# Optimization experiments

Measured on AMD Instinct MI355X. Metric: run time of the kernel, lower is better.

The kernel has to match this reference:

```python
import jax, jax.numpy as jnp
import numpy as np

HIDDEN = 2048
NUM_HEADS = 16
HEAD_DIM = HIDDEN // NUM_HEADS
WORLD_SIZE = 4
BATCH = 1
SEQ_SHARD = 2048


def setup_inputs() -> dict:
    key = jax.random.key(0)
    ks = jax.random.split(key, 9)
    s = 1.0 / np.sqrt(HIDDEN)
    return {
        'hidden_states': jax.random.normal(ks[0], (BATCH, SEQ_SHARD, HIDDEN), jnp.float32),
        'wq': jax.random.normal(ks[1], (HIDDEN, HIDDEN), jnp.float32) * s,
        'bq': jax.random.normal(ks[2], (HIDDEN,), jnp.float32) * s,
        'wk': jax.random.normal(ks[3], (HIDDEN, HIDDEN), jnp.float32) * s,
        'bk': jax.random.normal(ks[4], (HIDDEN,), jnp.float32) * s,
        'wv': jax.random.normal(ks[5], (HIDDEN, HIDDEN), jnp.float32) * s,
        'bv': jax.random.normal(ks[6], (HIDDEN,), jnp.float32) * s,
        'wo': jax.random.normal(ks[7], (HIDDEN, HIDDEN), jnp.float32) * s,
        'bo': jax.random.normal(ks[8], (HIDDEN,), jnp.float32) * s,
    }


def _ring_attention(q, k, v):
    # q, k, v: [B, H, S, D]. Simulation: every ring step receives the SAME
    # local KV shard (all_k_shards are clones of k), accumulated with
    # flash-style online softmax across WORLD_SIZE steps.
    B, H, S, D = q.shape
    scale = 1.0 / np.sqrt(D)
    output_acc = jnp.zeros_like(q)
    max_score = jnp.full((B, H, S, 1), -jnp.inf, dtype=q.dtype)
    sum_exp = jnp.zeros((B, H, S, 1), dtype=q.dtype)
    for _ in range(WORLD_SIZE):  # fixed small loop over ring steps
        scores = jnp.einsum('bhsd,bhtd->bhst', q, k) * scale  # [B,H,S,S]
        new_max = jnp.max(scores, axis=-1, keepdims=True)
        combined_max = jnp.maximum(max_score, new_max)
        old_scale = jnp.exp(max_score - combined_max)
        new_scale = jnp.exp(new_max - combined_max)
        new_exp = jnp.exp(scores - new_max)
        sum_exp = sum_exp * old_scale + jnp.sum(new_exp, axis=-1, keepdims=True) * new_scale
        output_acc = output_acc * old_scale + jnp.einsum('bhst,bhtd->bhsd', new_exp, v) * new_scale
        max_score = combined_max
    return output_acc / sum_exp


def reference(hidden_states, wq, bq, wk, bk, wv, bv, wo, bo):
    B, S, _ = hidden_states.shape
    # nn.Linear: y = x @ W^T + b
    q = hidden_states @ wq.T + bq
    k = hidden_states @ wk.T + bk
    v = hidden_states @ wv.T + bv
    split = lambda t: t.reshape(B, S, NUM_HEADS, HEAD_DIM).transpose(0, 2, 1, 3)
    attn = _ring_attention(split(q), split(k), split(v))  # [B,H,S,D]
    attn = attn.transpose(0, 2, 1, 3).reshape(B, S, HIDDEN)
    return attn @ wo.T + bo
```

## Files before the change

kernel.cpp:

```cpp
#include <hip/hip_runtime.h>
#include <hip/hip_bf16.h>
#include <stdint.h>

#define SEQ 2048
#define HID 2048
#define NH 16
#define HD 128
#define QSCALE_L2E 0.1275304429019769f

typedef __attribute__((ext_vector_type(4))) float f32x4;
typedef __attribute__((ext_vector_type(8))) short short8;
typedef __attribute__((ext_vector_type(4))) float f4;
typedef __attribute__((ext_vector_type(4))) unsigned short us4;

__device__ __forceinline__ unsigned short f2bu(float f) {
  union { float f; unsigned int u; } c; c.f = f;
  unsigned int u = c.u + 0x7fffu + ((c.u >> 16) & 1u);
  return (unsigned short)(u >> 16);
}

__device__ __forceinline__ unsigned short f2bu_fast(float f) {
  union { float f; unsigned int u; } c; c.f = f;
  return (unsigned short)((c.u + 0x8000u) >> 16);
}

__device__ __forceinline__ float b2f(unsigned short u) {
  union { unsigned int u; float f; } c; c.u = ((unsigned int)u) << 16; return c.f;
}

__device__ __forceinline__ float exp2fast(float x) {
  float r; asm("v_exp_f32 %0, %1" : "=v"(r) : "v"(x)); return r;
}

__device__ __forceinline__ void gload_lds16(const void* g, void* l) {
  __builtin_amdgcn_global_load_lds((const __attribute__((address_space(1))) void*)g,
                                   (__attribute__((address_space(3))) void*)l, 16, 0, 0);
}

#define BAR() __builtin_amdgcn_s_barrier()
#define LGKM0() do { asm volatile("s_waitcnt lgkmcnt(0)" ::: "memory"); __builtin_amdgcn_sched_barrier(0); } while (0)
#define VM6()   do { asm volatile("s_waitcnt vmcnt(6)"   ::: "memory"); __builtin_amdgcn_sched_barrier(0); } while (0)
#define VM8()   do { asm volatile("s_waitcnt vmcnt(8)"   ::: "memory"); __builtin_amdgcn_sched_barrier(0); } while (0)
#define VM0()   do { asm volatile("s_waitcnt vmcnt(0)"   ::: "memory"); __builtin_amdgcn_sched_barrier(0); } while (0)

__global__ __launch_bounds__(256) void cvt_kernel(
    const float* __restrict__ s0, const float* __restrict__ s1,
    const float* __restrict__ s2, const float* __restrict__ s3,
    const float* __restrict__ s4,
    unsigned short* __restrict__ d0, unsigned short* __restrict__ d1,
    unsigned short* __restrict__ d2, unsigned short* __restrict__ d3,
    unsigned short* __restrict__ d4, int n)
{
  const float* s; unsigned short* d;
  switch (blockIdx.y) {
    case 0: s = s0; d = d0; break;
    case 1: s = s1; d = d1; break;
    case 2: s = s2; d = d2; break;
    case 3: s = s3; d = d3; break;
    default: s = s4; d = d4; break;
  }
  const int stride = gridDim.x * blockDim.x;
  for (int i = blockIdx.x * blockDim.x + threadIdx.x; i * 8 < n; i += stride) {
    f4 v0 = *(const f4*)&s[i * 8];
    f4 v1 = *(const f4*)&s[i * 8 + 4];
    short8 o;
    o[0] = (short)f2bu(v0[0]); o[1] = (short)f2bu(v0[1]);
    o[2] = (short)f2bu(v0[2]); o[3] = (short)f2bu(v0[3]);
    o[4] = (short)f2bu(v1[0]); o[5] = (short)f2bu(v1[1]);
    o[6] = (short)f2bu(v1[2]); o[7] = (short)f2bu(v1[3]);
    *(short8*)&d[i * 8] = o;
  }
}

template<int MODE>
__global__ __launch_bounds__(256, 3) void gemm97(
    const unsigned short* __restrict__ A,
    const unsigned short* __restrict__ B,
    const float* __restrict__ b0, const float* __restrict__ b1, const float* __restrict__ b2,
    unsigned short* __restrict__ O0, unsigned short* __restrict__ O1, unsigned short* __restrict__ O2,
    float* __restrict__ Of, int M, int N, int K)
{
  extern __shared__ unsigned short lds[];
  const int tid = threadIdx.x;
  const int lane = tid & 63, w = tid >> 6;
  const int g = lane >> 4, q = lane & 15;
  const int wgM = w >> 1, wgN = w & 1;
  const long bm = (long)blockIdx.y * 128, bn = (long)blockIdx.x * 128;
  const int NK = K >> 6;

  const int srl = lane >> 3;
  const int scE = ((lane & 7) ^ srl) * 8;
  const int c0 = (g ^ (q & 7)) * 8;
  const int c1 = c0 ^ 32;
  const int aB = (wgM * 64 + q) * 64;
  const int bB = (wgN * 64 + q) * 64;

  f32x4 acc[4][4] = {};
  short8 a[4][2], b[4][2];

#define STAGE(gp, gbase, jj, ldsOff) do {                                     \
    _Pragma("unroll")                                                         \
    for (int c_ = 0; c_ < 4; ++c_) {                                          \
      const long row_ = (c_ * 4 + w) * 8 + srl;                               \
      gload_lds16(&(gp)[((gbase) + row_) * (long)K + (jj) * 64 + scE],        \
                  &lds[(ldsOff) + (c_ * 4 + w) * 512]);                       \
    }                                                                         \
  } while (0)

#define QUADD(n0, n1)                                                         \
  do {                                                                        \
    __builtin_amdgcn_s_setprio(1);                                            \
    _Pragma("unroll")                                                         \
    for (int mi_ = 0; mi_ < 4; ++mi_) {                                       \
      acc[mi_][n0] = __builtin_amdgcn_mfma_f32_16x16x32_bf16(                 \
          a[mi_][0], b[n0][0], acc[mi_][n0], 0, 0, 0);                        \
      acc[mi_][n0] = __builtin_amdgcn_mfma_f32_16x16x32_bf16(                 \
          a[mi_][1], b[n0][1], acc[mi_][n0], 0, 0, 0);                        \
      acc[mi_][n1] = __builtin_amdgcn_mfma_f32_16x16x32_bf16(                 \
          a[mi_][0], b[n1][0], acc[mi_][n1], 0, 0, 0);                        \
      acc[mi_][n1] = __builtin_amdgcn_mfma_f32_16x16x32_bf16(                 \
          a[mi_][1], b[n1][1], acc[mi_][n1], 0, 0, 0);                        \
    }                                                                         \
    __builtin_amdgcn_s_setprio(0);                                            \
  } while (0)

  for (int j = 0; j < NK; ++j) {
    STAGE(A, bm, j, 0);
    STAGE(B, bn, j, 8192);
    VM0();
    BAR();
#pragma unroll
    for (int mi = 0; mi < 4; ++mi) {
      a[mi][0] = *(const short8*)&lds[aB + mi * 1024 + c0];
      a[mi][1] = *(const short8*)&lds[aB + mi * 1024 + c1];
    }
#pragma unroll
    for (int ni = 0; ni < 4; ++ni) {
      b[ni][0] = *(const short8*)&lds[8192 + bB + ni * 1024 + c0];
      b[ni][1] = *(const short8*)&lds[8192 + bB + ni * 1024 + c1];
    }
    QUADD(0, 1);
    QUADD(2, 3);
    BAR();
  }

#pragma unroll
  for (int ni = 0; ni < 4; ++ni) {
    const int col = (int)bn + wgN * 64 + ni * 16 + q;
    float bv;
    if (MODE == 4) {
      const int which = col >> 11, c = col & 2047;
      const float* bp = which == 0 ? b0 : (which == 1 ? b1 : b2);
      bv = bp[c];
    } else {
      bv = b0[col];
    }
#pragma unroll
    for (int mi = 0; mi < 4; ++mi)
#pragma unroll
      for (int r = 0; r < 4; ++r) {
        const long row = bm + wgM * 64 + mi * 16 + 4 * g + r;
        const float v = acc[mi][ni][r] + bv;
        if (MODE == 4) {
          const int which = col >> 11, c = col & 2047, head = c >> 7, d = c & 127;
          if (which == 0)      O0[((long)head * SEQ + row) * HD + d] = f2bu(v * QSCALE_L2E);
          else if (which == 1) O1[((long)head * SEQ + row) * HD + d] = f2bu(v);
          else                 O2[((long)head * HD + d) * SEQ + row] = f2bu(v);
        } else {
          Of[row * (long)N + col] = v;
        }
      }
  }
#undef STAGE
#undef QUADD
}

template<int MODE>
__global__ __launch_bounds__(256, 2) void gemm128(
    const unsigned short* __restrict__ A,
    const unsigned short* __restrict__ B,
    const float* __restrict__ b0, const float* __restrict__ b1, const float* __restrict__ b2,
    unsigned short* __restrict__ O0, unsigned short* __restrict__ O1, unsigned short* __restrict__ O2,
    float* __restrict__ Of, int M, int N, int K)
{
  constexpr int ASZ = 64 * 64;
  constexpr int BSZ = 128 * 64;

  extern __shared__ unsigned short lds[];
  const int tid = threadIdx.x;
  const int lane = tid & 63, w = tid >> 6;
  const int g = lane >> 4, q = lane & 15;
  const long bm = (long)blockIdx.y * 64, bn = (long)blockIdx.x * 128;
  const int NK = K >> 6;

  const int srl = lane >> 3;
  const int scE = ((lane & 7) ^ srl) * 8;
  const int c0 = (g ^ (q & 7)) * 8;
  const int c1 = c0 ^ 32;
  const int aB = q * 64;
  const int bB = (w * 32 + q) * 64;

  f32x4 acc[4][2] = {};
  short8 a[4][2], b[2][2];

#define STAGE_A(jj) do {                                                      \
    unsigned short* dst_ = lds + (((jj) & 1) ? ASZ : 0);                      \
    _Pragma("unroll")                                                         \
    for (int c_ = 0; c_ < 2; ++c_) {                                          \
      const long row_ = (c_ * 4 + w) * 8 + srl;                               \
      gload_lds16(&A[(bm + row_) * (long)K + (jj) * 64 + scE],                \
                  &dst_[(c_ * 4 + w) * 512]);                                 \
    }                                                                         \
  } while (0)

#define STAGE_B(jj) do {                                                      \
    unsigned short* dst_ = lds + 2 * ASZ + (((jj) & 1) ? BSZ : 0);            \
    _Pragma("unroll")                                                         \
    for (int c_ = 0; c_ < 4; ++c_) {                                          \
      const long row_ = (c_ * 4 + w) * 8 + srl;                               \
      gload_lds16(&B[(bn + row_) * (long)K + (jj) * 64 + scE],                \
                  &dst_[(c_ * 4 + w) * 512]);                                 \
    }                                                                         \
  } while (0)

#define QUAD8(ni)                                                             \
  do {                                                                        \
    __builtin_amdgcn_s_setprio(1);                                            \
    _Pragma("unroll")                                                         \
    for (int mi_ = 0; mi_ < 4; ++mi_) {                                       \
      acc[mi_][ni] = __builtin_amdgcn_mfma_f32_16x16x32_bf16(                 \
          a[mi_][0], b[ni][0], acc[mi_][ni], 0, 0, 0);                        \
      acc[mi_][ni] = __builtin_amdgcn_mfma_f32_16x16x32_bf16(                 \
          a[mi_][1], b[ni][1], acc[mi_][ni], 0, 0, 0);                        \
    }                                                                         \
    __builtin_amdgcn_s_setprio(0);                                            \
  } while (0)

  STAGE_A(0); STAGE_B(0);
  STAGE_A(1); STAGE_B(1);
  VM6();
  BAR();

  for (int j = 0; j < NK; ++j) {
    unsigned short* At = lds + ((j & 1) ? ASZ : 0);
    unsigned short* Bt = lds + 2 * ASZ + ((j & 1) ? BSZ : 0);

#pragma unroll
    for (int mi = 0; mi < 4; ++mi) {
      a[mi][0] = *(const short8*)&At[aB + mi * 1024 + c0];
      a[mi][1] = *(const short8*)&At[aB + mi * 1024 + c1];
    }
#pragma unroll
    for (int ni = 0; ni < 2; ++ni) {
      b[ni][0] = *(const short8*)&Bt[bB + ni * 1024 + c0];
      b[ni][1] = *(const short8*)&Bt[bB + ni * 1024 + c1];
    }
    QUAD8(0);
    LGKM0();
    BAR();
    if (j + 2 < NK) { STAGE_A(j + 2); STAGE_B(j + 2); }
    QUAD8(1);
    if (j < NK - 2) { VM6(); } else { VM0(); }
    BAR();
  }

#pragma unroll
  for (int ni = 0; ni < 2; ++ni) {
    const int col = (int)bn + w * 32 + ni * 16 + q;
    float bv;
    if (MODE == 4) {
      const int which = col >> 11, c = col & 2047;
      const float* bp = which == 0 ? b0 : (which == 1 ? b1 : b2);
      bv = bp[c];
    } else {
      bv = b0[col];
    }
#pragma unroll
    for (int mi = 0; mi < 4; ++mi)
#pragma unroll
      for (int r = 0; r < 4; ++r) {
        const long row = bm + mi * 16 + 4 * g + r;
        const float v = acc[mi][ni][r] + bv;
        if (MODE == 4) {
          const int which = col >> 11, c = col & 2047, head = c >> 7, d = c & 127;
          if (which == 0)      O0[((long)head * SEQ + row) * HD + d] = f2bu(v * QSCALE_L2E);
          else if (which == 1) O1[((long)head * SEQ + row) * HD + d] = f2bu(v);
          else                 O2[((long)head * HD + d) * SEQ + row] = f2bu(v);
        } else {
          Of[row * (long)N + col] = v;
        }
      }
  }
#undef STAGE_A
#undef STAGE_B
#undef QUAD8
}

#define KVB 64
__global__ __launch_bounds__(256) void flash_attn(
    const unsigned short* __restrict__ Qb,
    const unsigned short* __restrict__ Kb,
    const unsigned short* __restrict__ VTb,
    unsigned short* __restrict__ attnb)
{
  extern __shared__ unsigned short S[];
  const int tid = threadIdx.x;
  const int l = tid & 63, w = tid >> 6;
  const int g = l >> 4, q = l & 15;
  const int bid = blockIdx.x;
  const int jj = bid >> 3;
  const int h = ((bid & 7) << 1) | (jj >> 5);
  const int qb = jj & 31;
  const int qrow0 = qb * 64 + w * 16;

  unsigned short* Pw = S + 32768 + w * 1024;

  short8 qf[4];
#pragma unroll
  for (int dc = 0; dc < 4; ++dc)
    qf[dc] = *(const short8*)&Qb[((long)h * SEQ + qrow0 + q) * HD + dc * 32 + g * 8];

  f32x4 oacc[8] = {};
  float lsum[4] = {0.f, 0.f, 0.f, 0.f};

  const unsigned short* Kg = Kb + (long)h * SEQ * HD;
  const unsigned short* Vg = VTb + (long)h * HD * SEQ;

  const int kce = ((l & 15) ^ (l >> 4)) * 8;
  const int kco = kce ^ 32;
  const int vce = ((l & 7) ^ ((l >> 3) & 7)) * 8;
  const int krl = l >> 4;
  const int vrl = l >> 3;

  unsigned short* KdB = S + w * 2048;
  unsigned short* VdB = S + 16384 + w * 2048;

#define STAGE(kb_, bufsel) do {                                               \
    const unsigned short* Kp_ = Kg + (long)((kb_) + w * 16 + krl) * HD;       \
    const unsigned short* Vp_ = Vg + (long)(w * 32 + vrl) * SEQ + (kb_) + vce;\
    unsigned short* Kd_ = KdB + (bufsel) * 8192;                              \
    unsigned short* Vd_ = VdB + (bufsel) * 8192;                              \
    gload_lds16(Kp_ + 0 * 4 * HD + kce, Kd_ + 0 * 512);                       \
    gload_lds16(Kp_ + 1 * 4 * HD + kco, Kd_ + 1 * 512);                       \
    gload_lds16(Kp_ + 2 * 4 * HD + kce, Kd_ + 2 * 512);                       \
    gload_lds16(Kp_ + 3 * 4 * HD + kco, Kd_ + 3 * 512);                       \
    gload_lds16(Vp_ + 0 * 8 * SEQ, Vd_ + 0 * 512);                            \
    gload_lds16(Vp_ + 1 * 8 * SEQ, Vd_ + 1 * 512);                            \
    gload_lds16(Vp_ + 2 * 8 * SEQ, Vd_ + 2 * 512);                            \
    gload_lds16(Vp_ + 3 * 8 * SEQ, Vd_ + 3 * 512);                            \
  } while (0)

  STAGE(0, 0);
  STAGE(KVB, 1);
  VM8();
  BAR();

  for (int t = 0; t < 32; ++t) {
    const unsigned short* Kt = S + (t & 1) * 8192;
    const unsigned short* Vt = S + 16384 + (t & 1) * 8192;

    f32x4 sacc[4] = {};
    __builtin_amdgcn_s_setprio(1);
#pragma unroll
    for (int kc = 0; kc < 4; ++kc) {
      const int krow = kc * 16 + q;
      const int sw = (krow & 7) << 4;
#pragma unroll
      for (int dc = 0; dc < 4; ++dc) {
        short8 kf = *(const short8*)&Kt[((krow * 256 + dc * 64 + g * 16) ^ sw) >> 1];
        sacc[kc] = __builtin_amdgcn_mfma_f32_16x16x32_bf16(qf[dc], kf, sacc[kc], 0, 0, 0);
      }
    }
    __builtin_amdgcn_s_setprio(0);

    float p[4][4];
#pragma unroll
    for (int r = 0; r < 4; ++r) {
#pragma unroll
      for (int kc = 0; kc < 4; ++kc) p[kc][r] = exp2fast(sacc[kc][r]);
      lsum[r] += (p[0][r] + p[1][r]) + (p[2][r] + p[3][r]);
    }

#pragma unroll
    for (int r = 0; r < 4; ++r) {
      const int prow = 4 * g + r;
      const int sw = (prow & 7) << 4;
#pragma unroll
      for (int kc = 0; kc < 4; ++kc)
        Pw[((prow * 128 + (kc * 16 + q) * 2) ^ sw) >> 1] = f2bu_fast(p[kc][r]);
    }

    short8 pf[2];
    const int psw = (q & 7) << 4;
#pragma unroll
    for (int ks = 0; ks < 2; ++ks)
      pf[ks] = *(const short8*)&Pw[((q * 128 + ks * 64 + g * 16) ^ psw) >> 1];
    __builtin_amdgcn_s_setprio(1);
#pragma unroll
    for (int dt = 0; dt < 8; ++dt) {
      const int vrow = dt * 16 + q;
#pragma unroll
      for (int ks = 0; ks < 2; ++ks) {
        short8 vf = *(const short8*)&Vt[((vrow * 128 + ks * 64 + g * 16) ^ psw) >> 1];
        oacc[dt] = __builtin_amdgcn_mfma_f32_16x16x32_bf16(pf[ks], vf, oacc[dt], 0, 0, 0);
      }
    }
    __builtin_amdgcn_s_setprio(0);

    BAR();
    if (t + 2 < 32) STAGE((t + 2) * KVB, t & 1);
    if (t < 30) { VM8(); } else { VM0(); }
    BAR();
  }

#pragma unroll
  for (int off = 1; off < 16; off <<= 1)
#pragma unroll
    for (int r = 0; r < 4; ++r) lsum[r] += __shfl_xor(lsum[r], off);

  const float rl0 = 1.f / lsum[0], rl1 = 1.f / lsum[1];
  const float rl2 = 1.f / lsum[2], rl3 = 1.f / lsum[3];
#pragma unroll
  for (int dt = 0; dt < 8; ++dt) {
    const long colb = (long)h * HD + dt * 16 + q;
    attnb[(long)(qrow0 + 4 * g + 0) * HID + colb] = f2bu(oacc[dt][0] * rl0);
    attnb[(long)(qrow0 + 4 * g + 1) * HID + colb] = f2bu(oacc[dt][1] * rl1);
    attnb[(long)(qrow0 + 4 * g + 2) * HID + colb] = f2bu(oacc[dt][2] * rl2);
    attnb[(long)(qrow0 + 4 * g + 3) * HID + colb] = f2bu(oacc[dt][3] * rl3);
  }
#undef STAGE
}

extern "C" void kernel_launch(void* const* d_in, const int* in_sizes, int n_in,
                              void* d_out, int out_size, void* d_ws, size_t ws_size,
                              hipStream_t stream)
{
  const float* x  = (const float*)d_in[0];
  const float* wq = (const float*)d_in[1];
  const float* bq = (const float*)d_in[2];
  const float* wk = (const float*)d_in[3];
  const float* bk = (const float*)d_in[4];
  const float* wv = (const float*)d_in[5];
  const float* bv = (const float*)d_in[6];
  const float* wo = (const float*)d_in[7];
  const float* bo = (const float*)d_in[8];

  const long NEL = (long)HID * HID;
  unsigned short* Xb   = (unsigned short*)d_ws;
  unsigned short* Wqkv = Xb + NEL;
  unsigned short* Wob  = Wqkv + 3 * NEL;
  unsigned short* Qbuf = Wob + NEL;
  unsigned short* Kbuf = Qbuf + NEL;
  unsigned short* VTb  = Kbuf + NEL;
  unsigned short* Attn = VTb + NEL;

  static bool attrDone = false;
  if (!attrDone) {
    hipFuncSetAttribute(reinterpret_cast<const void*>(flash_attn),
                        hipFuncAttributeMaxDynamicSharedMemorySize, 73728);
    attrDone = true;
  }

  cvt_kernel<<<dim3(512, 5), 256, 0, stream>>>(
      x, wq, wk, wv, wo, Xb, Wqkv, Wqkv + NEL, Wqkv + 2 * NEL, Wob, (int)NEL);

  gemm97<4><<<dim3(48, 16), 256, 32768, stream>>>(
      Xb, Wqkv, bq, bk, bv, Qbuf, Kbuf, VTb, nullptr, SEQ, 3 * HID, HID);

  flash_attn<<<dim3(512), 256, 73728, stream>>>(Qbuf, Kbuf, VTb, Attn);

  gemm128<3><<<dim3(16, 32), 256, 49152, stream>>>(
      Attn, Wob, bo, nullptr, nullptr, nullptr, nullptr, nullptr,
      (float*)d_out, SEQ, HID, HID);
}
```

Measured before the change: 164.0 us.

## Software-pipeline attention loop: overlap next tile's QK^T with current softmax and PV

The attention main loop is restructured into a two-stage software pipeline. The QK^T MFMAs for tile t+1 are issued before the exp, P-store and PV MFMAs for tile t, using ping-pong score accumulators. K and V staging is split so the K tile for t+2 is issued early and the V tile later, with the vmcnt waits retuned to match. The aim is to hide softmax and LDS latency behind matrix work, at the cost of extra VGPRs for the second score accumulator set, which may lower occupancy.

Result: no change. 161.7 us, median of 2 (-1.4%).

```diff
diff --git a/kernel.cpp b/kernel.cpp
--- a/kernel.cpp
+++ b/kernel.cpp
@@ -40,7 +40,7 @@
 #define BAR() __builtin_amdgcn_s_barrier()
 #define LGKM0() do { asm volatile("s_waitcnt lgkmcnt(0)" ::: "memory"); __builtin_amdgcn_sched_barrier(0); } while (0)
 #define VM6()   do { asm volatile("s_waitcnt vmcnt(6)"   ::: "memory"); __builtin_amdgcn_sched_barrier(0); } while (0)
-#define VM8()   do { asm volatile("s_waitcnt vmcnt(8)"   ::: "memory"); __builtin_amdgcn_sched_barrier(0); } while (0)
+#define VM4()   do { asm volatile("s_waitcnt vmcnt(4)"   ::: "memory"); __builtin_amdgcn_sched_barrier(0); } while (0)
 #define VM0()   do { asm volatile("s_waitcnt vmcnt(0)"   ::: "memory"); __builtin_amdgcn_sched_barrier(0); } while (0)
 
 __global__ __launch_bounds__(256) void cvt_kernel(
@@ -321,6 +321,8 @@
     qf[dc] = *(const short8*)&Qb[((long)h * SEQ + qrow0 + q) * HD + dc * 32 + g * 8];
 
   f32x4 oacc[8] = {};
+  f32x4 saccA[4], saccB[4];
+  const f32x4 zero4 = {};
   float lsum[4] = {0.f, 0.f, 0.f, 0.f};
 
   const unsigned short* Kg = Kb + (long)h * SEQ * HD;
@@ -331,86 +333,104 @@
   const int vce = ((l & 7) ^ ((l >> 3) & 7)) * 8;
   const int krl = l >> 4;
   const int vrl = l >> 3;
-
   unsigned short* KdB = S + w * 2048;
   unsigned short* VdB = S + 16384 + w * 2048;
 
-#define STAGE(kb_, bufsel) do {                                               \
+#define STAGE_K(kb_, bufsel) do {                                             \
     const unsigned short* Kp_ = Kg + (long)((kb_) + w * 16 + krl) * HD;       \
-    const unsigned short* Vp_ = Vg + (long)(w * 32 + vrl) * SEQ + (kb_) + vce;\
     unsigned short* Kd_ = KdB + (bufsel) * 8192;                              \
-    unsigned short* Vd_ = VdB + (bufsel) * 8192;                              \
     gload_lds16(Kp_ + 0 * 4 * HD + kce, Kd_ + 0 * 512);                       \
     gload_lds16(Kp_ + 1 * 4 * HD + kco, Kd_ + 1 * 512);                       \
     gload_lds16(Kp_ + 2 * 4 * HD + kce, Kd_ + 2 * 512);                       \
     gload_lds16(Kp_ + 3 * 4 * HD + kco, Kd_ + 3 * 512);                       \
+  } while (0)
+
+#define STAGE_V(kb_, bufsel) do {                                             \
+    const unsigned short* Vp_ = Vg + (long)(w * 32 + vrl) * SEQ + (kb_) + vce;\
+    unsigned short* Vd_ = VdB + (bufsel) * 8192;                              \
     gload_lds16(Vp_ + 0 * 8 * SEQ, Vd_ + 0 * 512);                            \
     gload_lds16(Vp_ + 1 * 8 * SEQ, Vd_ + 1 * 512);                            \
     gload_lds16(Vp_ + 2 * 8 * SEQ, Vd_ + 2 * 512);                            \
     gload_lds16(Vp_ + 3 * 8 * SEQ, Vd_ + 3 * 512);                            \
   } while (0)
 
-  STAGE(0, 0);
-  STAGE(KVB, 1);
-  VM8();
+#define QKT(T1, SN) do {                                                      \
+    const unsigned short* Kt_ = S + ((T1) & 1) * 8192;                        \
+    __builtin_amdgcn_s_setprio(1);                                            \
+    _Pragma("unroll")                                                         \
+    for (int kc = 0; kc < 4; ++kc) {                                          \
+      const int krow_ = kc * 16 + q;                                          \
+      const int sw_ = (krow_ & 7) << 4;                                       \
+      _Pragma("unroll")                                                       \
+      for (int dc = 0; dc < 4; ++dc) {                                        \
+        short8 kf_ = *(const short8*)&Kt_[((krow_ * 256 + dc * 64 + g * 16) ^ sw_) >> 1]; \
+        SN[kc] = __builtin_amdgcn_mfma_f32_16x16x32_bf16(qf[dc], kf_, SN[kc], 0, 0, 0);   \
+      }                                                                       \
+    }                                                                         \
+    __builtin_amdgcn_s_setprio(0);                                            \
+  } while (0)
+
+#define FINISH_PV(T, SC) do {                                                 \
+    float p_[4][4];                                                           \
+    _Pragma("unroll")                                                         \
+    for (int r = 0; r < 4; ++r) {                                             \
+      _Pragma("unroll")                                                       \
+      for (int kc = 0; kc < 4; ++kc) p_[kc][r] = exp2fast(SC[kc][r]);         \
+      lsum[r] += (p_[0][r] + p_[1][r]) + (p_[2][r] + p_[3][r]);               \
+    }                                                                         \
+    _Pragma("unroll")                                                         \
+    for (int r = 0; r < 4; ++r) {                                             \
+      const int prow_ = 4 * g + r;                                            \
+      const int sw_ = (prow_ & 7) << 4;                                       \
+      _Pragma("unroll")                                                       \
+      for (int kc = 0; kc < 4; ++kc)                                          \
+        Pw[((prow_ * 128 + (kc * 16 + q) * 2) ^ sw_) >> 1] = f2bu_fast(p_[kc][r]); \
+    }                                                                         \
+    short8 pf_[2];                                                            \
+    const int psw_ = (q & 7) << 4;                                            \
+    _Pragma("unroll")                                                         \
+    for (int ks = 0; ks < 2; ++ks)                                            \
+      pf_[ks] = *(const short8*)&Pw[((q * 128 + ks * 64 + g * 16) ^ psw_) >> 1]; \
+    const unsigned short* Vt_ = S + 16384 + ((T) & 1) * 8192;                 \
+    __builtin_amdgcn_s_setprio(1);                                            \
+    _Pragma("unroll")                                                         \
+    for (int dt = 0; dt < 8; ++dt) {                                          \
+      const int vrow_ = dt * 16 + q;                                          \
+      _Pragma("unroll")                                                       \
+      for (int ks = 0; ks < 2; ++ks) {                                        \
+        short8 vf_ = *(const short8*)&Vt_[((vrow_ * 128 + ks * 64 + g * 16) ^ psw_) >> 1]; \
+        oacc[dt] = __builtin_amdgcn_mfma_f32_16x16x32_bf16(pf_[ks], vf_, oacc[dt], 0, 0, 0); \
+      }                                                                       \
+    }                                                                         \
+    __builtin_amdgcn_s_setprio(0);                                            \
+  } while (0)
+
+#define PHASE(T, SC, SN) do {                                                 \
+    if ((T) + 2 < 32) STAGE_K(((T) + 2) * KVB, (T) & 1);                      \
+    if ((T) + 1 < 32) {                                                       \
+      _Pragma("unroll")                                                       \
+      for (int kc = 0; kc < 4; ++kc) SN[kc] = zero4;                          \
+      QKT((T) + 1, SN);                                                       \
+    }                                                                         \
+    FINISH_PV(T, SC);                                                         \
+    BAR();                                                                    \
+    if ((T) + 2 < 32) STAGE_V(((T) + 2) * KVB, (T) & 1);                      \
+    if ((T) <= 29) { VM4(); } else { VM0(); }                                 \
+    BAR();                                                                    \
+  } while (0)
+
+  STAGE_K(0, 0); STAGE_V(0, 0);
+  STAGE_K(KVB, 1); STAGE_V(KVB, 1);
+  VM0();
   BAR();
-
-  for (int t = 0; t < 32; ++t) {
-    const unsigned short* Kt = S + (t & 1) * 8192;
-    const unsigned short* Vt = S + 16384 + (t & 1) * 8192;
-
-    f32x4 sacc[4] = {};
-    __builtin_amdgcn_s_setprio(1);
-#pragma unroll
-    for (int kc = 0; kc < 4; ++kc) {
-      const int krow = kc * 16 + q;
-      const int sw = (krow & 7) << 4;
-#pragma unroll
-      for (int dc = 0; dc < 4; ++dc) {
-        short8 kf = *(const short8*)&Kt[((krow * 256 + dc * 64 + g * 16) ^ sw) >> 1];
-        sacc[kc] = __builtin_amdgcn_mfma_f32_16x16x32_bf16(qf[dc], kf, sacc[kc], 0, 0, 0);
-      }
-    }
-    __builtin_amdgcn_s_setprio(0);
-
-    float p[4][4];
-#pragma unroll
-    for (int r = 0; r < 4; ++r) {
-#pragma unroll
-      for (int kc = 0; kc < 4; ++kc) p[kc][r] = exp2fast(sacc[kc][r]);
-      lsum[r] += (p[0][r] + p[1][r]) + (p[2][r] + p[3][r]);
-    }
-
-#pragma unroll
-    for (int r = 0; r < 4; ++r) {
-      const int prow = 4 * g + r;
-      const int sw = (prow & 7) << 4;
-#pragma unroll
-      for (int kc = 0; kc < 4; ++kc)
-        Pw[((prow * 128 + (kc * 16 + q) * 2) ^ sw) >> 1] = f2bu_fast(p[kc][r]);
-    }
-
-    short8 pf[2];
-    const int psw = (q & 7) << 4;
-#pragma unroll
-    for (int ks = 0; ks < 2; ++ks)
-      pf[ks] = *(const short8*)&Pw[((q * 128 + ks * 64 + g * 16) ^ psw) >> 1];
-    __builtin_amdgcn_s_setprio(1);
-#pragma unroll
-    for (int dt = 0; dt < 8; ++dt) {
-      const int vrow = dt * 16 + q;
-#pragma unroll
-      for (int ks = 0; ks < 2; ++ks) {
-        short8 vf = *(const short8*)&Vt[((vrow * 128 + ks * 64 + g * 16) ^ psw) >> 1];
-        oacc[dt] = __builtin_amdgcn_mfma_f32_16x16x32_bf16(pf[ks], vf, oacc[dt], 0, 0, 0);
-      }
-    }
-    __builtin_amdgcn_s_setprio(0);
-
-    BAR();
-    if (t + 2 < 32) STAGE((t + 2) * KVB, t & 1);
-    if (t < 30) { VM8(); } else { VM0(); }
-    BAR();
+#pragma unroll
+  for (int kc = 0; kc < 4; ++kc) saccA[kc] = zero4;
+  QKT(0, saccA);
+  BAR();
+
+  for (int t = 0; t < 32; t += 2) {
+    PHASE(t, saccA, saccB);
+    PHASE(t + 1, saccB, saccA);
   }
 
 #pragma unroll
@@ -428,7 +448,11 @@
     attnb[(long)(qrow0 + 4 * g + 2) * HID + colb] = f2bu(oacc[dt][2] * rl2);
     attnb[(long)(qrow0 + 4 * g + 3) * HID + colb] = f2bu(oacc[dt][3] * rl3);
   }
-#undef STAGE
+#undef STAGE_K
+#undef STAGE_V
+#undef QKT
+#undef FINISH_PV
+#undef PHASE
 }
 
 extern "C" void kernel_launch(void* const* d_in, const int* in_sizes, int n_in,
```
